# Performance work log

Measured on AMD Instinct MI355X. Metric: run time of the kernel, lower is better.

## Reference

```python
import jax, jax.numpy as jnp
import numpy as np

T, F, H = 2048, 256, 384  # seq_len, input_size, hidden_size


def setup_inputs() -> dict:
    key = jax.random.key(0)
    ks = jax.random.split(key, 16)
    s = 1.0 / np.sqrt(F)
    d = {"x": jax.random.normal(ks[0], (T, F), jnp.float32)}
    names = ["q", "k", "v", "i", "f", "o"]
    for j, n in enumerate(names):
        d[f"W{n}"] = jax.random.uniform(ks[1 + j], (H, F), jnp.float32, -s, s)
        d[f"b{n}"] = jax.random.uniform(ks[7 + j], (H,), jnp.float32, -s, s)
    d["conv_w"] = jax.random.uniform(ks[13], (1, 1, 4), jnp.float32, -0.5, 0.5)
    d["conv_b"] = jax.random.uniform(ks[14], (1,), jnp.float32, -0.5, 0.5)
    return d


def _forward(x, Wq, bq, Wk, bk, Wv, bv, Wi, bi, Wf, bf, Wo, bo, conv_w, conv_b):
    # Conv1d(1->1, kernel=4, padding=(3,3)) along time, per input feature.
    xt = x.T[:, None, :]  # (F, 1, T)  feature axis acts as batch
    y = jax.lax.conv_general_dilated(xt, conv_w, (1,), [(3, 3)])  # (F, 1, T+3)
    xp = (y[:, 0, :] + conv_b[0]).T  # (T+3, F)

    inv_sqrt_h = 1.0 / jnp.sqrt(jnp.asarray(H, xp.dtype))
    # Precompute all per-step projections with dense GEMMs (time-parallel part).
    q = xp @ Wq.T + bq                      # (T+3, H)
    k = (xp @ Wk.T + bk) * inv_sqrt_h       # (T+3, H); extra bias_k is zero-init
    v = xp @ Wv.T + bv
    i = jnp.exp(xp @ Wi.T + bi)
    f = jax.nn.sigmoid(xp @ Wf.T + bf)
    o = jax.nn.sigmoid(xp @ Wo.T + bo)

    def step(carry, inp):
        C, n = carry                         # C: (H,H), n: (H,)
        qt, kt, vt, it, ft, ot = inp
        C = ft * C + it * jnp.outer(vt, kt)  # broadcast over last axis, as original
        n = ft * n + it * kt
        den = jnp.maximum(jnp.abs(jnp.dot(n, qt)), 1.0)
        h = ot * (C @ qt) / den
        return (C, n), h

    init = (jnp.zeros((H, H), xp.dtype), jnp.zeros((H,), xp.dtype))
    _, hs = jax.lax.scan(step, init, (q, k, v, i, f, o))
    return hs[-1]  # return_all=False -> last hidden state, shape (H,)


def reference(x, Wq, bq, Wk, bk, Wv, bv, Wi, bi, Wf, bf, Wo, bo, conv_w, conv_b):
    return _forward(x, Wq, bq, Wk, bk, Wv, bv, Wi, bi, Wf, bf, Wo, bo, conv_w, conv_b)
```

## Files before the change

### kernel.cpp

```cpp
#include <hip/hip_runtime.h>
#include <math.h>

#define T_IN 2048
#define TP   2051
#define F    256
#define H    384
#define BK   16
#define BT2  32
#define NT2  65
#define NCS  257
#define NC3  257

__device__ __forceinline__ float logsig(float z) {
    return (z >= 0.0f) ? -log1pf(__expf(-z)) : z - log1pf(__expf(z));
}

union F4 { float4 v; float f[4]; };

__global__ __launch_bounds__(256) void k1_conv(const float* __restrict__ x,
                        const float* __restrict__ cw,
                        const float* __restrict__ cb, float* __restrict__ xp) {
    int t = blockIdx.x * 4 + (threadIdx.x >> 6);
    int f4 = threadIdx.x & 63;
    if (t >= TP) return;
    float w[4] = {cw[0], cw[1], cw[2], cw[3]};
    float b = cb[0];
    float4 acc = {b, b, b, b};
    int i0 = t - 3;
    const float4* x4 = (const float4*)x;
    #pragma unroll
    for (int j = 0; j < 4; ++j) {
        int tt = i0 + j;
        if (tt >= 0 && tt < T_IN) {
            float4 xv = x4[tt * 64 + f4];
            acc.x = fmaf(w[j], xv.x, acc.x);
            acc.y = fmaf(w[j], xv.y, acc.y);
            acc.z = fmaf(w[j], xv.z, acc.z);
            acc.w = fmaf(w[j], xv.w, acc.w);
        }
    }
    ((float4*)xp)[t * 64 + f4] = acc;
}

__global__ __launch_bounds__(256) void k2_proj(
    const float* __restrict__ xp,
    const float* __restrict__ Wk, const float* __restrict__ bk,
    const float* __restrict__ Wi, const float* __restrict__ bi,
    const float* __restrict__ Wf, const float* __restrict__ bf,
    float* __restrict__ zk, float* __restrict__ ai, float* __restrict__ lf,
    float* __restrict__ cs) {
    __shared__ float alds[2][BT2][20];
    __shared__ float wlds[2][BK][66];
    __shared__ float csred[8][66];
    int tid = threadIdx.x;
    int mz = blockIdx.z;
    const float* __restrict__ W    = (mz == 0) ? Wk : (mz == 1) ? Wi : Wf;
    const float* __restrict__ bias = (mz == 0) ? bk : (mz == 1) ? bi : bf;
    int t0 = blockIdx.x * BT2, b0 = blockIdx.y * 64;
    int tx = tid & 31, ty = tid >> 5;
    float2 acc[4];
    #pragma unroll
    for (int u = 0; u < 4; ++u) { acc[u].x = 0.f; acc[u].y = 0.f; }

    int wrow = tid >> 2;
    int wk4 = (tid & 3) * 4;
    int grow = (b0 + wrow) * 256 + wk4;
    int atq = tid >> 2;
    int arow = (t0 + atq) * 256 + wk4;
    bool aval = (tid < 128) && (t0 + atq < TP);

    float4 aw = {0.f, 0.f, 0.f, 0.f};
    float4 ww;
    if (aval) aw = *(const float4*)&xp[arow];
    ww = *(const float4*)&W[grow];

    for (int i = 0; i < 16; ++i) {
        int buf = i & 1;
        if (tid < 128) *(float4*)&alds[buf][atq][wk4] = aw;
        {
            F4 wu; wu.v = ww;
            #pragma unroll
            for (int j = 0; j < 4; ++j)
                wlds[buf][wk4 + j][wrow] = wu.f[j];
        }
        __syncthreads();
        if (i < 15) {
            int k0 = (i + 1) * BK;
            if (aval) aw = *(const float4*)&xp[arow + k0];
            ww = *(const float4*)&W[grow + k0];
        }
        #pragma unroll
        for (int g = 0; g < 4; ++g) {
            F4 av0, av1, av2, av3;
            av0.v = *(const float4*)&alds[buf][4 * ty + 0][4 * g];
            av1.v = *(const float4*)&alds[buf][4 * ty + 1][4 * g];
            av2.v = *(const float4*)&alds[buf][4 * ty + 2][4 * g];
            av3.v = *(const float4*)&alds[buf][4 * ty + 3][4 * g];
            #pragma unroll
            for (int j = 0; j < 4; ++j) {
                float2 w0 = *(const float2*)&wlds[buf][4 * g + j][2 * tx];
                acc[0].x = fmaf(av0.f[j], w0.x, acc[0].x);
                acc[0].y = fmaf(av0.f[j], w0.y, acc[0].y);
                acc[1].x = fmaf(av1.f[j], w0.x, acc[1].x);
                acc[1].y = fmaf(av1.f[j], w0.y, acc[1].y);
                acc[2].x = fmaf(av2.f[j], w0.x, acc[2].x);
                acc[2].y = fmaf(av2.f[j], w0.y, acc[2].y);
                acc[3].x = fmaf(av3.f[j], w0.x, acc[3].x);
                acc[3].y = fmaf(av3.f[j], w0.y, acc[3].y);
            }
        }
    }
    int bA = b0 + 2 * tx;
    float2 b2 = *(const float2*)&bias[bA];
    if (mz == 0) {
        const float sc = 0.05103103630798287f;
        #pragma unroll
        for (int u = 0; u < 4; ++u) {
            int t = t0 + 4 * ty + u;
            if (t < TP) {
                float2 v;
                v.x = (acc[u].x + b2.x) * sc; v.y = (acc[u].y + b2.y) * sc;
                *(float2*)&zk[t * H + bA] = v;
            }
        }
    } else if (mz == 1) {
        #pragma unroll
        for (int u = 0; u < 4; ++u) {
            int t = t0 + 4 * ty + u;
            if (t < TP) {
                float2 v;
                v.x = acc[u].x + b2.x; v.y = acc[u].y + b2.y;
                *(float2*)&ai[t * H + bA] = v;
            }
        }
    } else {
        float2 lsum = {0.f, 0.f};
        #pragma unroll
        for (int u = 0; u < 4; ++u) {
            int t = t0 + 4 * ty + u;
            if (t < TP) {
                float2 l2;
                l2.x = logsig(acc[u].x + b2.x);
                l2.y = logsig(acc[u].y + b2.y);
                *(float2*)&lf[t * H + bA] = l2;
                lsum.x += l2.x; lsum.y += l2.y;
            }
        }
        *(float2*)&csred[ty][2 * tx] = lsum;
        __syncthreads();
        int cl = tid >> 6;
        int bb = tid & 63;
        int c = blockIdx.x * 4 + cl;
        if (c < NCS)
            cs[c * H + b0 + bb] = csred[2 * cl][bb] + csred[2 * cl + 1][bb];
    }
}

__global__ __launch_bounds__(256) void k2b_qo(const float* __restrict__ xp,
        const float* __restrict__ Wq, const float* __restrict__ bq,
        const float* __restrict__ Wo, const float* __restrict__ bo,
        float* __restrict__ q, float* __restrict__ o) {
    int tid = threadIdx.x;
    int lane = tid & 63;
    int row = blockIdx.x * 4 + (tid >> 6);
    float4 xv = *(const float4*)&xp[(TP - 1) * 256 + lane * 4];
    float4 q4 = *(const float4*)&Wq[row * 256 + lane * 4];
    float4 o4 = *(const float4*)&Wo[row * 256 + lane * 4];
    float aq = fmaf(xv.x, q4.x, fmaf(xv.y, q4.y, fmaf(xv.z, q4.z, xv.w * q4.w)));
    float ao = fmaf(xv.x, o4.x, fmaf(xv.y, o4.y, fmaf(xv.z, o4.z, xv.w * o4.w)));
    #pragma unroll
    for (int off = 32; off; off >>= 1) {
        aq += __shfl_down(aq, off, 64);
        ao += __shfl_down(ao, off, 64);
    }
    if (lane == 0) {
        q[row] = aq + bq[row];
        o[row] = 1.0f / (1.0f + __expf(-(ao + bo[row])));
    }
}

__global__ __launch_bounds__(64) void k3b_scan(const float* __restrict__ cs,
                                               float* __restrict__ co) {
    int b = blockIdx.x * 64 + threadIdx.x;
    float L = 0.0f;
    #pragma unroll 16
    for (int c = NCS - 1; c >= 0; --c) {
        co[c * H + b] = L;
        L += cs[c * H + b];
    }
}

__global__ __launch_bounds__(384) void k3_fused(
    const float* __restrict__ ai, const float* __restrict__ lf,
    const float* __restrict__ zk, const float* __restrict__ co,
    const float* __restrict__ q, const float* __restrict__ xp,
    float* __restrict__ zf, float* __restrict__ Gf) {
    __shared__ float zred[6][256];
    __shared__ float gred[6];
    int tid = threadIdx.x;
    int w = tid >> 6, lane = tid & 63;
    int c = blockIdx.x, ts = c * 8;
    float co0 = co[c * H + tid];
    float qb = q[tid];
    float aiv[8], lfv[8], zkv[8];
    float4 xv[8];
    if (ts + 8 <= TP) {
        #pragma unroll
        for (int u = 0; u < 8; ++u) {
            int idx = (ts + u) * H + tid;
            aiv[u] = ai[idx]; lfv[u] = lf[idx]; zkv[u] = zk[idx];
            xv[u] = *(const float4*)&xp[(ts + u) * 256 + lane * 4];
        }
    } else {
        #pragma unroll
        for (int u = 0; u < 8; ++u) {
            if (ts + u < TP) {
                int idx = (ts + u) * H + tid;
                aiv[u] = ai[idx]; lfv[u] = lf[idx]; zkv[u] = zk[idx];
                xv[u] = *(const float4*)&xp[(ts + u) * 256 + lane * 4];
            } else {
                aiv[u] = -1e30f; lfv[u] = 0.f; zkv[u] = 0.f;
                xv[u].x = xv[u].y = xv[u].z = xv[u].w = 0.f;
            }
        }
    }
    float S = 0.f, gsum = 0.f;
    float z0 = 0.f, z1 = 0.f, z2 = 0.f, z3 = 0.f;
    #pragma unroll
    for (int u = 7; u >= 0; --u) {
        float wv = __expf(aiv[u] + co0 + S) * zkv[u] * qb;
        S += lfv[u];
        float s = wv;
        s += __shfl_xor(s, 1, 64);
        s += __shfl_xor(s, 2, 64);
        s += __shfl_xor(s, 4, 64);
        s += __shfl_xor(s, 8, 64);
        s += __shfl_xor(s, 16, 64);
        s += __shfl_xor(s, 32, 64);
        gsum += s;
        z0 = fmaf(s, xv[u].x, z0);
        z1 = fmaf(s, xv[u].y, z1);
        z2 = fmaf(s, xv[u].z, z2);
        z3 = fmaf(s, xv[u].w, z3);
    }
    zred[w][lane * 4 + 0] = z0;
    zred[w][lane * 4 + 1] = z1;
    zred[w][lane * 4 + 2] = z2;
    zred[w][lane * 4 + 3] = z3;
    if (lane == 0) gred[w] = gsum;
    __syncthreads();
    if (tid < 256) {
        float s = zred[0][tid] + zred[1][tid] + zred[2][tid]
                + zred[3][tid] + zred[4][tid] + zred[5][tid];
        atomicAdd(&zf[tid], s);
    }
    if (tid == 0)
        atomicAdd(Gf, gred[0] + gred[1] + gred[2] + gred[3] + gred[4] + gred[5]);
}

__global__ __launch_bounds__(256) void k6_out(const float* __restrict__ zf,
        const float* __restrict__ Gf,
        const float* __restrict__ Wv, const float* __restrict__ bv,
        const float* __restrict__ o, float* __restrict__ out) {
    int tid = threadIdx.x;
    int lane = tid & 63;
    int row = blockIdx.x * 4 + (tid >> 6);
    float Gv = Gf[0];
    float4 zv = *(const float4*)&zf[lane * 4];
    float4 wv = *(const float4*)&Wv[row * 256 + lane * 4];
    float acc = fmaf(zv.x, wv.x, fmaf(zv.y, wv.y, fmaf(zv.z, wv.z, zv.w * wv.w)));
    #pragma unroll
    for (int off = 32; off; off >>= 1) acc += __shfl_down(acc, off, 64);
    if (lane == 0)
        out[row] = o[row] * (acc + bv[row] * Gv) / fmaxf(fabsf(Gv), 1.0f);
}

extern "C" void kernel_launch(void* const* d_in, const int* in_sizes, int n_in,
                              void* d_out, int out_size, void* d_ws, size_t ws_size,
                              hipStream_t stream) {
    const float* x  = (const float*)d_in[0];
    const float* Wq = (const float*)d_in[1];  const float* bq = (const float*)d_in[2];
    const float* Wk = (const float*)d_in[3];  const float* bk = (const float*)d_in[4];
    const float* Wv = (const float*)d_in[5];  const float* bv = (const float*)d_in[6];
    const float* Wi = (const float*)d_in[7];  const float* bi = (const float*)d_in[8];
    const float* Wf = (const float*)d_in[9];  const float* bf = (const float*)d_in[10];
    const float* Wo = (const float*)d_in[11]; const float* bo = (const float*)d_in[12];
    const float* cw = (const float*)d_in[13]; const float* cb = (const float*)d_in[14];
    float* out = (float*)d_out;

    float* ws = (float*)d_ws;
    float* xp  = ws;
    float* zk  = xp  + TP * F;
    float* ai  = zk  + TP * H;
    float* lf  = ai  + TP * H;
    float* cs  = lf  + TP * H;
    float* co  = cs  + NCS * H;
    float* qv  = co  + NCS * H;
    float* ov  = qv  + H;
    float* zf  = ov  + H;
    float* Gf  = zf  + F;

    hipMemsetAsync((void*)zf, 0, (F + 4) * sizeof(float), stream);
    k1_conv<<<(TP + 3) / 4, 256, 0, stream>>>(x, cw, cb, xp);
    k2b_qo<<<96, 256, 0, stream>>>(xp, Wq, bq, Wo, bo, qv, ov);
    k2_proj<<<dim3(NT2, 6, 3), 256, 0, stream>>>(xp, Wk, bk, Wi, bi, Wf, bf, zk, ai, lf, cs);
    k3b_scan<<<6, 64, 0, stream>>>(cs, co);
    k3_fused<<<NC3, 384, 0, stream>>>(ai, lf, zk, co, qv, xp, zf, Gf);
    k6_out<<<96, 256, 0, stream>>>(zf, Gf, Wv, bv, ov, out);
}
```

Before: 147.4 us.

## Fuse pipeline into three launches with last-block ticket epilogue

```diff
diff --git a/kernel.cpp b/kernel.cpp
--- a/kernel.cpp
+++ b/kernel.cpp
@@ -17,29 +17,61 @@
 
 union F4 { float4 v; float f[4]; };
 
-__global__ __launch_bounds__(256) void k1_conv(const float* __restrict__ x,
-                        const float* __restrict__ cw,
-                        const float* __restrict__ cb, float* __restrict__ xp) {
-    int t = blockIdx.x * 4 + (threadIdx.x >> 6);
-    int f4 = threadIdx.x & 63;
-    if (t >= TP) return;
-    float w[4] = {cw[0], cw[1], cw[2], cw[3]};
-    float b = cb[0];
-    float4 acc = {b, b, b, b};
-    int i0 = t - 3;
-    const float4* x4 = (const float4*)x;
-    #pragma unroll
-    for (int j = 0; j < 4; ++j) {
-        int tt = i0 + j;
-        if (tt >= 0 && tt < T_IN) {
-            float4 xv = x4[tt * 64 + f4];
-            acc.x = fmaf(w[j], xv.x, acc.x);
-            acc.y = fmaf(w[j], xv.y, acc.y);
-            acc.z = fmaf(w[j], xv.z, acc.z);
-            acc.w = fmaf(w[j], xv.w, acc.w);
-        }
-    }
-    ((float4*)xp)[t * 64 + f4] = acc;
+__global__ __launch_bounds__(256) void k1_front(const float* __restrict__ x,
+        const float* __restrict__ cw, const float* __restrict__ cb,
+        const float* __restrict__ Wq, const float* __restrict__ bq,
+        const float* __restrict__ Wo, const float* __restrict__ bo,
+        float* __restrict__ xp, float* __restrict__ q, float* __restrict__ o,
+        float* __restrict__ zf) {
+    int bid = blockIdx.x;
+    int tid = threadIdx.x;
+    if (bid < 513) {
+        int t = bid * 4 + (tid >> 6);
+        int f4 = tid & 63;
+        if (t >= TP) return;
+        float w[4] = {cw[0], cw[1], cw[2], cw[3]};
+        float b = cb[0];
+        float4 acc = {b, b, b, b};
+        int i0 = t - 3;
+        const float4* x4 = (const float4*)x;
+        #pragma unroll
+        for (int j = 0; j < 4; ++j) {
+            int tt = i0 + j;
+            if (tt >= 0 && tt < T_IN) {
+                float4 xv = x4[tt * 64 + f4];
+                acc.x = fmaf(w[j], xv.x, acc.x);
+                acc.y = fmaf(w[j], xv.y, acc.y);
+                acc.z = fmaf(w[j], xv.z, acc.z);
+                acc.w = fmaf(w[j], xv.w, acc.w);
+            }
+        }
+        ((float4*)xp)[t * 64 + f4] = acc;
+    } else if (bid < 609) {
+        int lane = tid & 63;
+        int row = (bid - 513) * 4 + (tid >> 6);
+        float w0 = cw[0], b = cb[0];
+        float4 xr = ((const float4*)x)[2047 * 64 + lane];
+        float4 xv;
+        xv.x = fmaf(w0, xr.x, b);
+        xv.y = fmaf(w0, xr.y, b);
+        xv.z = fmaf(w0, xr.z, b);
+        xv.w = fmaf(w0, xr.w, b);
+        float4 q4 = *(const float4*)&Wq[row * 256 + lane * 4];
+        float4 o4 = *(const float4*)&Wo[row * 256 + lane * 4];
+        float aq = fmaf(xv.x, q4.x, fmaf(xv.y, q4.y, fmaf(xv.z, q4.z, xv.w * q4.w)));
+        float ao = fmaf(xv.x, o4.x, fmaf(xv.y, o4.y, fmaf(xv.z, o4.z, xv.w * o4.w)));
+        #pragma unroll
+        for (int off = 32; off; off >>= 1) {
+            aq += __shfl_down(aq, off, 64);
+            ao += __shfl_down(ao, off, 64);
+        }
+        if (lane == 0) {
+            q[row] = aq + bq[row];
+            o[row] = 1.0f / (1.0f + __expf(-(ao + bo[row])));
+        }
+    } else {
+        for (int i = tid; i < 272; i += 256) zf[i] = 0.0f;
+    }
 }
 
 __global__ __launch_bounds__(256) void k2_proj(
@@ -156,51 +188,24 @@
     }
 }
 
-__global__ __launch_bounds__(256) void k2b_qo(const float* __restrict__ xp,
-        const float* __restrict__ Wq, const float* __restrict__ bq,
-        const float* __restrict__ Wo, const float* __restrict__ bo,
-        float* __restrict__ q, float* __restrict__ o) {
-    int tid = threadIdx.x;
-    int lane = tid & 63;
-    int row = blockIdx.x * 4 + (tid >> 6);
-    float4 xv = *(const float4*)&xp[(TP - 1) * 256 + lane * 4];
-    float4 q4 = *(const float4*)&Wq[row * 256 + lane * 4];
-    float4 o4 = *(const float4*)&Wo[row * 256 + lane * 4];
-    float aq = fmaf(xv.x, q4.x, fmaf(xv.y, q4.y, fmaf(xv.z, q4.z, xv.w * q4.w)));
-    float ao = fmaf(xv.x, o4.x, fmaf(xv.y, o4.y, fmaf(xv.z, o4.z, xv.w * o4.w)));
-    #pragma unroll
-    for (int off = 32; off; off >>= 1) {
-        aq += __shfl_down(aq, off, 64);
-        ao += __shfl_down(ao, off, 64);
-    }
-    if (lane == 0) {
-        q[row] = aq + bq[row];
-        o[row] = 1.0f / (1.0f + __expf(-(ao + bo[row])));
-    }
-}
-
-__global__ __launch_bounds__(64) void k3b_scan(const float* __restrict__ cs,
-                                               float* __restrict__ co) {
-    int b = blockIdx.x * 64 + threadIdx.x;
-    float L = 0.0f;
-    #pragma unroll 16
-    for (int c = NCS - 1; c >= 0; --c) {
-        co[c * H + b] = L;
-        L += cs[c * H + b];
-    }
-}
-
-__global__ __launch_bounds__(384) void k3_fused(
+__global__ __launch_bounds__(384) void k3_mega(
     const float* __restrict__ ai, const float* __restrict__ lf,
-    const float* __restrict__ zk, const float* __restrict__ co,
+    const float* __restrict__ zk, const float* __restrict__ cs,
     const float* __restrict__ q, const float* __restrict__ xp,
-    float* __restrict__ zf, float* __restrict__ Gf) {
+    float* __restrict__ zf, float* __restrict__ Gf,
+    unsigned int* __restrict__ ticket,
+    const float* __restrict__ Wv, const float* __restrict__ bv,
+    const float* __restrict__ o, float* __restrict__ out) {
     __shared__ float zred[6][256];
     __shared__ float gred[6];
+    __shared__ unsigned int stick;
+    __shared__ float sGv;
     int tid = threadIdx.x;
     int w = tid >> 6, lane = tid & 63;
     int c = blockIdx.x, ts = c * 8;
-    float co0 = co[c * H + tid];
+    float co0 = 0.0f;
+    #pragma unroll 8
+    for (int c2 = NCS - 1; c2 > c; --c2) co0 += cs[c2 * H + tid];
     float qb = q[tid];
     float aiv[8], lfv[8], zkv[8];
     float4 xv[8];
@@ -256,23 +261,33 @@
     }
     if (tid == 0)
         atomicAdd(Gf, gred[0] + gred[1] + gred[2] + gred[3] + gred[4] + gred[5]);
-}
-
-__global__ __launch_bounds__(256) void k6_out(const float* __restrict__ zf,
-        const float* __restrict__ Gf,
-        const float* __restrict__ Wv, const float* __restrict__ bv,
-        const float* __restrict__ o, float* __restrict__ out) {
-    int tid = threadIdx.x;
-    int lane = tid & 63;
-    int row = blockIdx.x * 4 + (tid >> 6);
-    float Gv = Gf[0];
-    float4 zv = *(const float4*)&zf[lane * 4];
-    float4 wv = *(const float4*)&Wv[row * 256 + lane * 4];
-    float acc = fmaf(zv.x, wv.x, fmaf(zv.y, wv.y, fmaf(zv.z, wv.z, zv.w * wv.w)));
-    #pragma unroll
-    for (int off = 32; off; off >>= 1) acc += __shfl_down(acc, off, 64);
-    if (lane == 0)
-        out[row] = o[row] * (acc + bv[row] * Gv) / fmaxf(fabsf(Gv), 1.0f);
+    __threadfence();
+    __syncthreads();
+    if (tid == 0) {
+        __threadfence();
+        stick = atomicAdd(ticket, 1u);
+    }
+    __syncthreads();
+    if (stick == NC3 - 1) {
+        if (tid == 0) sGv = atomicAdd(Gf, 0.0f);
+        __syncthreads();
+        float Gv = sGv;
+        float4 zv;
+        zv.x = atomicAdd(&zf[lane * 4 + 0], 0.0f);
+        zv.y = atomicAdd(&zf[lane * 4 + 1], 0.0f);
+        zv.z = atomicAdd(&zf[lane * 4 + 2], 0.0f);
+        zv.w = atomicAdd(&zf[lane * 4 + 3], 0.0f);
+        #pragma unroll 4
+        for (int r = 0; r < 64; ++r) {
+            int row = w * 64 + r;
+            float4 wv = *(const float4*)&Wv[row * 256 + lane * 4];
+            float acc = fmaf(zv.x, wv.x, fmaf(zv.y, wv.y, fmaf(zv.z, wv.z, zv.w * wv.w)));
+            #pragma unroll
+            for (int off = 32; off; off >>= 1) acc += __shfl_down(acc, off, 64);
+            if (lane == 0)
+                out[row] = o[row] * (acc + bv[row] * Gv) / fmaxf(fabsf(Gv), 1.0f);
+        }
+    }
 }
 
 extern "C" void kernel_launch(void* const* d_in, const int* in_sizes, int n_in,
@@ -299,12 +314,9 @@
     float* ov  = qv  + H;
     float* zf  = ov  + H;
     float* Gf  = zf  + F;
-
-    hipMemsetAsync((void*)zf, 0, (F + 4) * sizeof(float), stream);
-    k1_conv<<<(TP + 3) / 4, 256, 0, stream>>>(x, cw, cb, xp);
-    k2b_qo<<<96, 256, 0, stream>>>(xp, Wq, bq, Wo, bo, qv, ov);
+    unsigned int* tk = (unsigned int*)(zf + 264);
+
+    k1_front<<<610, 256, 0, stream>>>(x, cw, cb, Wq, bq, Wo, bo, xp, qv, ov, zf);
     k2_proj<<<dim3(NT2, 6, 3), 256, 0, stream>>>(xp, Wk, bk, Wi, bi, Wf, bf, zk, ai, lf, cs);
-    k3b_scan<<<6, 64, 0, stream>>>(cs, co);
-    k3_fused<<<NC3, 384, 0, stream>>>(ai, lf, zk, co, qv, xp, zf, Gf);
-    k6_out<<<96, 256, 0, stream>>>(zf, Gf, Wv, bv, ov, out);
-}
+    k3_mega<<<NC3, 384, 0, stream>>>(ai, lf, zk, cs, qv, xp, zf, Gf, tk, Wv, bv, ov, out);
+}
```

Result: slower. 212.1 us (+43.9%).
